# Performance work log

Measured on AMD Instinct MI355X. Metric: run time of the kernel, lower is better.

Reference implementation:

```python
import jax, jax.numpy as jnp
import numpy as np
from jax import lax

NB, HH, WW, C = 8, 64, 64, 192
G, K, DW_K, PA_K = 12, 3, 5, 3
GC, P = C // G, K * K
PAD, STRIDE, DIL = 1, 1, 1
OFFSET_SCALE = 1.0
LN_EPS = 1e-5


def _grid_sample(img, grid):
    # img: (B,Cc,H,W); grid: (B,L,P,2) xy in [-1,1]; bilinear, zeros padding, align_corners=False
    B, Cc, H, W = img.shape
    gx = (grid[..., 0] + 1.0) * (W * 0.5) - 0.5
    gy = (grid[..., 1] + 1.0) * (H * 0.5) - 0.5
    x0, y0 = jnp.floor(gx), jnp.floor(gy)

    def gather(xi, yi):
        valid = (xi >= 0) & (xi <= W - 1) & (yi >= 0) & (yi <= H - 1)
        xc = jnp.clip(xi, 0, W - 1).astype(jnp.int32)
        yc = jnp.clip(yi, 0, H - 1).astype(jnp.int32)
        v = jax.vmap(lambda im, y, x: im[:, y, x])(img, yc, xc)  # (B,Cc,L,P)
        return v * valid[:, None].astype(img.dtype)

    wx1, wy1 = gx - x0, gy - y0
    wx0, wy0 = 1.0 - wx1, 1.0 - wy1
    return (gather(x0, y0) * (wx0 * wy0)[:, None]
            + gather(x0 + 1.0, y0) * (wx1 * wy0)[:, None]
            + gather(x0, y0 + 1.0) * (wx0 * wy1)[:, None]
            + gather(x0 + 1.0, y0 + 1.0) * (wx1 * wy1)[:, None])


def _dcnv3_core(x, offset, mask):
    # x: (N,H,W,C) projected input; offset: (N,H,W,G*P*2); mask: (N,H,W,G*P)
    N, H, W, _ = x.shape
    xp = jnp.pad(x, ((0, 0), (PAD, PAD), (PAD, PAD), (0, 0)))
    Hp, Wp = H + 2 * PAD, W + 2 * PAD
    Ho, Wo = offset.shape[1], offset.shape[2]
    base = (DIL * (K - 1)) // 2 + 0.5
    ref_y = (base + jnp.arange(Ho) * STRIDE) / Hp
    ref_x = (base + jnp.arange(Wo) * STRIDE) / Wp
    ref = jnp.stack(jnp.broadcast_arrays(ref_x[None, :], ref_y[:, None]), -1)  # (Ho,Wo,2) xy
    start = -((DIL * (K - 1)) // 2)
    pts = (start + jnp.arange(K) * DIL).astype(x.dtype)
    gxg = jnp.broadcast_to((pts / Wp)[:, None], (K, K))  # w offset varies along dim0 (torch order)
    gyg = jnp.broadcast_to((pts / Hp)[None, :], (K, K))
    grid = jnp.tile(jnp.stack([gxg, gyg], -1).reshape(P, 2), (G, 1))  # (G*P,2)
    loc = ref[None, :, :, None, :] + grid * OFFSET_SCALE  # (1,Ho,Wo,G*P,2)
    norm = jnp.array([Wp, Hp], dtype=x.dtype)
    loc = loc + offset.reshape(N, Ho, Wo, G * P, 2) * OFFSET_SCALE / norm
    sg = 2.0 * loc - 1.0  # (N,Ho,Wo,G*P,2)
    img = xp.reshape(N, Hp * Wp, G, GC).transpose(0, 2, 3, 1).reshape(N * G, GC, Hp, Wp)
    grd = sg.reshape(N, Ho * Wo, G, P, 2).transpose(0, 2, 1, 3, 4).reshape(N * G, Ho * Wo, P, 2)
    samp = _grid_sample(img, grd)  # (N*G, GC, L, P)
    m = mask.reshape(N, Ho * Wo, G, P).transpose(0, 2, 1, 3).reshape(N * G, 1, Ho * Wo, P)
    out = (samp * m).sum(-1)  # (N*G, GC, L)
    return out.reshape(N, G, GC, Ho * Wo).transpose(0, 3, 1, 2).reshape(N, Ho, Wo, C)


def _dcnv3(x, dw_w, dw_b, ln_g, ln_b, off_w, off_b, msk_w, msk_b, in_w, in_b, out_w, out_b, cfs_w, cfs_b):
    N, H, W, _ = x.shape
    x_proj = x @ in_w + in_b
    # depthwise conv (5x5) -> LayerNorm (channels_last) -> GELU(exact)
    u = lax.conv_general_dilated(x, dw_w, (1, 1), 'SAME',
                                 dimension_numbers=('NHWC', 'HWIO', 'NHWC'),
                                 feature_group_count=C) + dw_b
    mu = u.mean(-1, keepdims=True)
    var = ((u - mu) ** 2).mean(-1, keepdims=True)
    u = (u - mu) * lax.rsqrt(var + LN_EPS) * ln_g + ln_b
    u = jax.nn.gelu(u, approximate=False)
    offset = u @ off_w + off_b  # (N,H,W,G*P*2)
    m = jax.nn.softmax((u @ msk_w + msk_b).reshape(N, H, W, G, P), axis=-1).reshape(N, H, W, G * P)
    y = _dcnv3_core(x_proj, offset, m)
    cfs = jax.nn.sigmoid(u @ cfs_w + cfs_b)  # (N,H,W,G)
    cfs = jnp.repeat(cfs, GC, axis=-1)       # (N,H,W,C), group-blockwise
    y = y * (1.0 - cfs) + x_proj * cfs
    return y @ out_w + out_b


def _patch_attention(x):
    # x: (N,H,W,C) -> std over softmax'd 3x3 neighbor scores: (N,H,W)
    N, H, W, _ = x.shape
    pad = (PA_K - 1) // 2
    xp = jnp.pad(x, ((0, 0), (pad, pad), (pad, pad), (0, 0)))
    neigh = jnp.stack([xp[:, i:i + H, j:j + W, :] for i in range(PA_K) for j in range(PA_K)],
                      axis=-1)  # (N,H,W,C,K1*K2), torch unfold ordering
    scores = jnp.einsum('nhwc,nhwck->nhwk', x, neigh)
    sm = jax.nn.softmax(scores, axis=-1)
    return jnp.std(sm, axis=-1, ddof=1)  # torch.std is unbiased


def setup_inputs() -> dict:
    key = jax.random.key(0)
    ks = jax.random.split(key, 8)
    s = 0.02
    return {
        'x': jax.random.normal(ks[0], (NB, HH, WW, C), jnp.float32),
        'dw_w': jax.random.normal(ks[1], (DW_K, DW_K, 1, C), jnp.float32) * s,
        'dw_b': jnp.zeros((C,), jnp.float32),
        'ln_g': jnp.ones((C,), jnp.float32),
        'ln_b': jnp.zeros((C,), jnp.float32),
        'off_w': jax.random.normal(ks[2], (C, G * P * 2), jnp.float32) * s,
        'off_b': jnp.zeros((G * P * 2,), jnp.float32),
        'msk_w': jax.random.normal(ks[3], (C, G * P), jnp.float32) * s,
        'msk_b': jnp.zeros((G * P,), jnp.float32),
        'in_w': jax.random.normal(ks[4], (C, C), jnp.float32) * s,
        'in_b': jnp.zeros((C,), jnp.float32),
        'out_w': jax.random.normal(ks[5], (C, C), jnp.float32) * s,
        'out_b': jnp.zeros((C,), jnp.float32),
        'cfs_w': jax.random.normal(ks[6], (C, G), jnp.float32) * s,
        'cfs_b': jnp.zeros((G,), jnp.float32),
    }


def reference(x, dw_w, dw_b, ln_g, ln_b, off_w, off_b, msk_w, msk_b, in_w, in_b, out_w, out_b, cfs_w, cfs_b):
    x1 = _dcnv3(x, dw_w, dw_b, ln_g, ln_b, off_w, off_b, msk_w, msk_b, in_w, in_b, out_w, out_b, cfs_w, cfs_b)
    mask = _patch_attention(x1)           # (N,H,W)
    return x + x1 * mask[..., None]
```

## Files before the change

### kernel.cpp

```cpp
#include <hip/hip_runtime.h>
#include <hip/hip_bf16.h>
#include <math.h>

#define NB 8
#define HH 64
#define WW 64
#define C 192
#define G 12
#define GC 16
#define P 9
#define NPIX (NB*HH*WW)

typedef __attribute__((ext_vector_type(8))) short short8;
typedef __attribute__((ext_vector_type(4))) float f32x4;
typedef unsigned short ushort;

__device__ __forceinline__ ushort to_bf16(float f) {
  __hip_bfloat16 b = __float2bfloat16(f);
  return *(ushort*)&b;
}
__device__ __forceinline__ float bf2f(ushort u) {
  union { unsigned u; float f; } cv; cv.u = ((unsigned)u) << 16; return cv.f;
}
__device__ __forceinline__ float bflo(unsigned u) {
  union { unsigned v; float f; } c; c.v = u << 16; return c.f;
}
__device__ __forceinline__ float bfhi(unsigned u) {
  union { unsigned v; float f; } c; c.v = u & 0xffff0000u; return c.f;
}

__global__ __launch_bounds__(256) void cvt_kernel(const float* __restrict__ in,
                                                  ushort* __restrict__ out) {
  int i = blockIdx.x*256 + threadIdx.x;
  float4 v0 = ((const float4*)in)[2*i];
  float4 v1 = ((const float4*)in)[2*i+1];
  short8 r;
  r[0]=to_bf16(v0.x); r[1]=to_bf16(v0.y); r[2]=to_bf16(v0.z); r[3]=to_bf16(v0.w);
  r[4]=to_bf16(v1.x); r[5]=to_bf16(v1.y); r[6]=to_bf16(v1.z); r[7]=to_bf16(v1.w);
  ((short8*)out)[i] = r;
}

__global__ void prep_w_kernel(const float* __restrict__ in_w, const float* __restrict__ out_w,
    const float* __restrict__ off_w, const float* __restrict__ msk_w, const float* __restrict__ cfs_w,
    const float* __restrict__ off_b, const float* __restrict__ msk_b, const float* __restrict__ cfs_b,
    ushort* __restrict__ in_wt, ushort* __restrict__ out_wt, ushort* __restrict__ wf_t,
    float* __restrict__ bf_bias) {
  int idx = blockIdx.x*256 + threadIdx.x;
  if (idx < 36864) {
    int n = idx/192, k = idx%192;
    in_wt[idx] = to_bf16(in_w[k*192 + n]);
  } else if (idx < 73728) {
    int j = idx - 36864; int n = j/192, k = j%192;
    out_wt[j] = to_bf16(out_w[k*192 + n]);
  } else if (idx < 147456) {
    int j = idx - 73728; int n = j/192, k = j%192;
    float v = 0.f;
    if (n < 216)      v = off_w[k*216 + n];
    else if (n < 324) v = msk_w[k*108 + (n-216)];
    else if (n < 336) v = cfs_w[k*12  + (n-324)];
    wf_t[j] = to_bf16(v);
  }
  if (idx < 384) {
    float b = 0.f;
    if (idx < 216)      b = off_b[idx];
    else if (idx < 324) b = msk_b[idx-216];
    else if (idx < 336) b = cfs_b[idx-324];
    bf_bias[idx] = b;
  }
}

template<int NW, int NSTORE, bool BF16OUT>
__global__ __launch_bounds__(256) void mfma_gemm(const ushort* __restrict__ A,
    const ushort* __restrict__ Wt, const float* __restrict__ bias,
    void* __restrict__ Cout_) {
  __shared__ ushort As[4*128*8];
  __shared__ ushort Bs[4*64*8];
  int pix0 = blockIdx.x * 128, n0 = blockIdx.y * 64;
  int tid = threadIdx.x;
  int wid = tid >> 6, lane = tid & 63;
  int lr = lane >> 4, lc = lane & 15;

  f32x4 acc[2][4];
  #pragma unroll
  for (int m=0;m<2;m++)
    #pragma unroll
    for (int j=0;j<4;j++) acc[m][j] = (f32x4){0.f,0.f,0.f,0.f};

  int sa0_kb = tid >> 7,        sa0_row = tid & 127;
  int sa1_kb = (tid+256) >> 7,  sa1_row = (tid+256) & 127;
  int sb_kb  = tid >> 6,        sb_n    = tid & 63;

  short8 pa0, pa1, pb;
  auto load_tile = [&](int k0) {
    pa0 = *(const short8*)&A[(size_t)(pix0 + sa0_row)*192 + k0 + sa0_kb*8];
    pa1 = *(const short8*)&A[(size_t)(pix0 + sa1_row)*192 + k0 + sa1_kb*8];
    pb  = *(const short8*)&Wt[(size_t)(n0 + sb_n)*192 + k0 + sb_kb*8];
  };
  load_tile(0);

  for (int t = 0; t < 6; t++) {
    __syncthreads();
    *(short8*)&As[(size_t)tid*8]        = pa0;
    *(short8*)&As[(size_t)(tid+256)*8]  = pa1;
    *(short8*)&Bs[(size_t)tid*8]        = pb;
    __syncthreads();
    if (t < 5) load_tile((t+1)*32);
    short8 a0 = *(const short8*)&As[(size_t)(lr*128 + wid*32 + lc)*8];
    short8 a1 = *(const short8*)&As[(size_t)(lr*128 + wid*32 + 16 + lc)*8];
    #pragma unroll
    for (int j=0;j<4;j++) {
      short8 b = *(const short8*)&Bs[(size_t)(lr*64 + j*16 + lc)*8];
      acc[0][j] = __builtin_amdgcn_mfma_f32_16x16x32_bf16(a0, b, acc[0][j], 0,0,0);
      acc[1][j] = __builtin_amdgcn_mfma_f32_16x16x32_bf16(a1, b, acc[1][j], 0,0,0);
    }
  }
  #pragma unroll
  for (int j=0;j<4;j++) {
    int col = n0 + j*16 + lc;
    if (NW != NSTORE && col >= NSTORE) continue;
    float bb = bias[col];
    #pragma unroll
    for (int m=0;m<2;m++) {
      size_t rbase = pix0 + wid*32 + m*16 + lr*4;
      #pragma unroll
      for (int r=0;r<4;r++) {
        float v = acc[m][j][r] + bb;
        if (BF16OUT) ((ushort*)Cout_)[(rbase + r)*NSTORE + col] = to_bf16(v);
        else         ((float*) Cout_)[(rbase + r)*NSTORE + col] = v;
      }
    }
  }
}

#define SEG 16
__global__ __launch_bounds__(192) void dw_ln_gelu_kernel(const float* __restrict__ x,
    const float* __restrict__ dw_w, const float* __restrict__ dw_b,
    const float* __restrict__ ln_g, const float* __restrict__ ln_b,
    ushort* __restrict__ u_out) {
  int blk = blockIdx.x;
  int qw = blk & 3; int nh = blk >> 2;
  int h = nh & 63, n = nh >> 6;
  int c = threadIdx.x;
  int w0 = qw * SEG;

  float kw[25];
  #pragma unroll
  for (int t=0;t<25;t++) kw[t] = dw_w[t*C + c];

  float acc[SEG];
  float bb = dw_b[c];
  #pragma unroll
  for (int i=0;i<SEG;i++) acc[i] = bb;

  #pragma unroll
  for (int i=0;i<5;i++) {
    int hy = h + i - 2;
    if (hy < 0 || hy >= HH) continue;
    const float* rowp = &x[(((size_t)n*HH + hy)*WW)*C + c];
    #pragma unroll
    for (int wi=0; wi<SEG+4; wi++) {
      int w_in = w0 - 2 + wi;
      if (w_in < 0 || w_in >= WW) continue;
      float v = rowp[(size_t)w_in*C];
      #pragma unroll
      for (int j=0;j<5;j++) {
        int a = wi - j;
        if (a >= 0 && a < SEG) acc[a] += v * kw[i*5+j];
      }
    }
  }

  __shared__ float lds_acc[SEG][C+1];
  __shared__ float part1[SEG][12], part2[SEG][12];
  __shared__ float mu_s[SEG], rs_s[SEG];
  #pragma unroll
  for (int i=0;i<SEG;i++) lds_acc[i][c] = acc[i];
  __syncthreads();
  {
    int p = threadIdx.x & 15, chunk = threadIdx.x >> 4;
    float s1 = 0.f, s2 = 0.f;
    #pragma unroll
    for (int k=0;k<16;k++) {
      float v = lds_acc[p][chunk*16 + k];
      s1 += v; s2 += v*v;
    }
    part1[p][chunk] = s1; part2[p][chunk] = s2;
  }
  __syncthreads();
  if (threadIdx.x < SEG) {
    int p = threadIdx.x;
    float t1 = 0.f, t2 = 0.f;
    #pragma unroll
    for (int k=0;k<12;k++){ t1 += part1[p][k]; t2 += part2[p][k]; }
    float mu = t1 * (1.0f/C);
    float var = t2 * (1.0f/C) - mu*mu;
    mu_s[p] = mu; rs_s[p] = rsqrtf(var + 1e-5f);
  }
  __syncthreads();
  float gg = ln_g[c], lb = ln_b[c];
  size_t obase = ((size_t)nh*WW + w0)*C + c;
  #pragma unroll
  for (int i=0;i<SEG;i++) {
    float uv = (acc[i] - mu_s[i])*rs_s[i]*gg + lb;
    uv = 0.5f*uv*(1.0f + erff(uv*0.70710678118654752f));
    u_out[obase + (size_t)i*C] = to_bf16(uv);
  }
}

#define SPX 4
__global__ __launch_bounds__(192) void sample_kernel(const ushort* __restrict__ omc,
    const ushort* __restrict__ x_proj, ushort* __restrict__ y_out) {
  int pix0 = blockIdx.x * SPX;
  int n = pix0 >> 12;
  int hw = pix0 & 4095; int h = hw >> 6; int w0 = hw & 63;
  int tid = threadIdx.x;
  __shared__ int   addrs[SPX*108*4];
  __shared__ float wts[SPX*108*4];
  __shared__ float msm[SPX][108];
  __shared__ float cfss[SPX][12];

  for (int i = tid; i < SPX*108; i += 192) {
    int px = i / 108, gp = i % 108;
    int p = gp % 9;
    const float pts[3] = {-1.f, 0.f, 1.f};
    unsigned off2 = ((const unsigned*)omc)[(size_t)(pix0+px)*168 + gp];
    float ox = bflo(off2), oy = bfhi(off2);
    float gx = 1.0f + (float)(w0+px) + pts[p/3] + ox;
    float gy = 1.0f + (float)h + pts[p%3] + oy;
    float x0f = floorf(gx), y0f = floorf(gy);
    float wx1 = gx - x0f, wy1 = gy - y0f;
    float wx0 = 1.f-wx1, wy0 = 1.f-wy1;
    int x0 = (int)x0f, y0 = (int)y0f;
    bool xv0 = (x0   >= 1) && (x0   <= 64);
    bool xv1 = (x0+1 >= 1) && (x0+1 <= 64);
    bool yv0 = (y0   >= 1) && (y0   <= 64);
    bool yv1 = (y0+1 >= 1) && (y0+1 <= 64);
    int base = n*HH*WW*C;
    int4 a4;
    a4.x = (yv0&&xv0) ? (base + ((y0-1)*WW + (x0-1))*C)*2 : 0;
    a4.y = (yv0&&xv1) ? (base + ((y0-1)*WW + (x0  ))*C)*2 : 0;
    a4.z = (yv1&&xv0) ? (base + ((y0  )*WW + (x0-1))*C)*2 : 0;
    a4.w = (yv1&&xv1) ? (base + ((y0  )*WW + (x0  ))*C)*2 : 0;
    ((int4*)addrs)[i] = a4;
    float4 w4;
    w4.x = (yv0&&xv0) ? wx0*wy0 : 0.f;
    w4.y = (yv0&&xv1) ? wx1*wy0 : 0.f;
    w4.z = (yv1&&xv0) ? wx0*wy1 : 0.f;
    w4.w = (yv1&&xv1) ? wx1*wy1 : 0.f;
    ((float4*)wts)[i] = w4;
  }
  if (tid < SPX*12) {
    int px = tid / 12, gg = tid % 12;
    const ushort* mrow = &omc[(size_t)(pix0+px)*336 + 216 + gg*9];
    float lv[P];
    #pragma unroll
    for (int p=0;p<P;p++) lv[p] = bf2f(mrow[p]);
    float m = -1e30f;
    #pragma unroll
    for (int p=0;p<P;p++) m = fmaxf(m, lv[p]);
    float e[P]; float s = 0.f;
    #pragma unroll
    for (int p=0;p<P;p++){ e[p] = expf(lv[p]-m); s += e[p]; }
    float inv = 1.0f/s;
    #pragma unroll
    for (int p=0;p<P;p++) msm[px][gg*9+p] = e[p]*inv;
  } else if (tid < SPX*12*2) {
    int q = tid - SPX*12;
    int px = q / 12, gg = q % 12;
    cfss[px][gg] = 1.0f/(1.0f+expf(-bf2f(omc[(size_t)(pix0+px)*336 + 324 + gg])));
  }
  __syncthreads();
  for (int i = tid; i < SPX*108; i += 192) {
    int px = i / 108, gp = i % 108;
    float m = msm[px][gp] * (1.0f - cfss[px][gp/9]);
    f32x4 w4 = *(f32x4*)&wts[i*4];
    w4 *= m;
    *(f32x4*)&wts[i*4] = w4;
  }
  __syncthreads();
  int px = tid / 48, s = tid - (tid/48)*48;
  int g = s >> 2;
  int cb = s * 8;
  const char* xb = (const char*)x_proj;
  float4 accY = {0.f,0.f,0.f,0.f};
  #pragma unroll
  for (int pb = 0; pb < 3; pb++) {
    uint2 q0_, q1_, q2_, q3_, q4_, q5_, q6_, q7_, q8_, q9_, qa_, qb_;
    float4 wv0, wv1, wv2;
    {
      int gp = g*9 + pb*3;
      int4 a0 = ((const int4*)addrs)[px*108+gp];
      int4 a1 = ((const int4*)addrs)[px*108+gp+1];
      int4 a2 = ((const int4*)addrs)[px*108+gp+2];
      wv0 = ((const float4*)wts)[px*108+gp];
      wv1 = ((const float4*)wts)[px*108+gp+1];
      wv2 = ((const float4*)wts)[px*108+gp+2];
      q0_ = *(const uint2*)(xb + (unsigned)(a0.x + cb));
      q1_ = *(const uint2*)(xb + (unsigned)(a0.y + cb));
      q2_ = *(const uint2*)(xb + (unsigned)(a0.z + cb));
      q3_ = *(const uint2*)(xb + (unsigned)(a0.w + cb));
      q4_ = *(const uint2*)(xb + (unsigned)(a1.x + cb));
      q5_ = *(const uint2*)(xb + (unsigned)(a1.y + cb));
      q6_ = *(const uint2*)(xb + (unsigned)(a1.z + cb));
      q7_ = *(const uint2*)(xb + (unsigned)(a1.w + cb));
      q8_ = *(const uint2*)(xb + (unsigned)(a2.x + cb));
      q9_ = *(const uint2*)(xb + (unsigned)(a2.y + cb));
      qa_ = *(const uint2*)(xb + (unsigned)(a2.z + cb));
      qb_ = *(const uint2*)(xb + (unsigned)(a2.w + cb));
    }
    accY.x += wv0.x*bflo(q0_.x) + wv0.y*bflo(q1_.x) + wv0.z*bflo(q2_.x) + wv0.w*bflo(q3_.x);
    accY.y += wv0.x*bfhi(q0_.x) + wv0.y*bfhi(q1_.x) + wv0.z*bfhi(q2_.x) + wv0.w*bfhi(q3_.x);
    accY.z += wv0.x*bflo(q0_.y) + wv0.y*bflo(q1_.y) + wv0.z*bflo(q2_.y) + wv0.w*bflo(q3_.y);
    accY.w += wv0.x*bfhi(q0_.y) + wv0.y*bfhi(q1_.y) + wv0.z*bfhi(q2_.y) + wv0.w*bfhi(q3_.y);
    accY.x += wv1.x*bflo(q4_.x) + wv1.y*bflo(q5_.x) + wv1.z*bflo(q6_.x) + wv1.w*bflo(q7_.x);
    accY.y += wv1.x*bfhi(q4_.x) + wv1.y*bfhi(q5_.x) + wv1.z*bfhi(q6_.x) + wv1.w*bfhi(q7_.x);
    accY.z += wv1.x*bflo(q4_.y) + wv1.y*bflo(q5_.y) + wv1.z*bflo(q6_.y) + wv1.w*bflo(q7_.y);
    accY.w += wv1.x*bfhi(q4_.y) + wv1.y*bfhi(q5_.y) + wv1.z*bfhi(q6_.y) + wv1.w*bfhi(q7_.y);
    accY.x += wv2.x*bflo(q8_.x) + wv2.y*bflo(q9_.x) + wv2.z*bflo(qa_.x) + wv2.w*bflo(qb_.x);
    accY.y += wv2.x*bfhi(q8_.x) + wv2.y*bfhi(q9_.x) + wv2.z*bfhi(qa_.x) + wv2.w*bfhi(qb_.x);
    accY.z += wv2.x*bflo(q8_.y) + wv2.y*bflo(q9_.y) + wv2.z*bflo(qa_.y) + wv2.w*bflo(qb_.y);
    accY.w += wv2.x*bfhi(q8_.y) + wv2.y*bfhi(q9_.y) + wv2.z*bfhi(qa_.y) + wv2.w*bfhi(qb_.y);
  }
  float cf = cfss[px][g];
  uint2 qx = *(const uint2*)(xb + ((size_t)(pix0+px)*C)*2 + cb);
  accY.x += bflo(qx.x)*cf;
  accY.y += bfhi(qx.x)*cf;
  accY.z += bflo(qx.y)*cf;
  accY.w += bfhi(qx.y)*cf;
  ushort4 r;
  r.x = to_bf16(accY.x); r.y = to_bf16(accY.y);
  r.z = to_bf16(accY.z); r.w = to_bf16(accY.w);
  *(ushort4*)&y_out[(size_t)(pix0+px)*C + s*4] = r;
}

__global__ __launch_bounds__(256) void pattn_kernel(const float* __restrict__ x,
    const ushort* __restrict__ x1, float* __restrict__ out) {
  __shared__ unsigned xs[100*97];
  __shared__ float psc[64][36];
  __shared__ float sd_s[64];
  int blk = blockIdx.x;
  int n = blk >> 6;
  int ty = (blk >> 3) & 7, tx = blk & 7;
  int th0 = ty*8, tw0 = tx*8;
  int tid = threadIdx.x;
  const unsigned* x1u = (const unsigned*)x1;
  for (int i = tid; i < 100*96; i += 256) {
    int cell = i / 96, wd = i - cell*96;
    int gy = th0 - 1 + cell/10, gx = tw0 - 1 + cell%10;
    unsigned v = 0;
    if (gy>=0 && gy<HH && gx>=0 && gx<WW)
      v = x1u[(((size_t)n*HH+gy)*WW+gx)*96 + wd];
    xs[cell*97 + wd] = v;
  }
  __syncthreads();
  {
    int px = tid >> 2, qq = tid & 3;
    int py = px >> 3, pxx = px & 7;
    int cell = (py+1)*10 + (pxx+1);
    float cen[48];
    #pragma unroll
    for (int k=0;k<24;k++) {
      unsigned w = xs[cell*97 + qq*24 + k];
      cen[2*k] = bflo(w); cen[2*k+1] = bfhi(w);
    }
    #pragma unroll
    for (int ni=0;ni<9;ni++) {
      int nc = cell + (ni/3-1)*10 + (ni%3-1);
      float a = 0.f;
      #pragma unroll
      for (int k=0;k<24;k++) {
        unsigned w = xs[nc*97 + qq*24 + k];
        a += cen[2*k]*bflo(w) + cen[2*k+1]*bfhi(w);
      }
      psc[px][qq*9+ni] = a;
    }
  }
  __syncthreads();
  if (tid < 64) {
    float sc[9];
    #pragma unroll
    for (int k=0;k<9;k++)
      sc[k] = psc[tid][k] + psc[tid][9+k] + psc[tid][18+k] + psc[tid][27+k];
    float m = sc[0];
    #pragma unroll
    for (int k=1;k<9;k++) m = fmaxf(m, sc[k]);
    float pr[9]; float s = 0.f;
    #pragma unroll
    for (int k=0;k<9;k++){ pr[k] = expf(sc[k]-m); s += pr[k]; }
    float inv = 1.0f/s;
    float mean = 0.f;
    #pragma unroll
    for (int k=0;k<9;k++){ pr[k] *= inv; mean += pr[k]; }
    mean *= (1.0f/9.0f);
    float var = 0.f;
    #pragma unroll
    for (int k=0;k<9;k++){ float d = pr[k]-mean; var += d*d; }
    sd_s[tid] = sqrtf(var*(1.0f/8.0f));
  }
  __syncthreads();
  for (int i = tid; i < 64*96; i += 256) {
    int p2 = i / 96, wd = i - p2*96;
    int py2 = p2 >> 3, px2 = p2 & 7;
    unsigned v = xs[((py2+1)*10 + (px2+1))*97 + wd];
    size_t pix = ((size_t)n*HH + th0+py2)*WW + tw0+px2;
    float2 xv = ((const float2*)x)[pix*96 + wd];
    float sd = sd_s[p2];
    float2 o; o.x = xv.x + bflo(v)*sd; o.y = xv.y + bfhi(v)*sd;
    ((float2*)out)[pix*96 + wd] = o;
  }
}

extern "C" void kernel_launch(void* const* d_in, const int* in_sizes, int n_in,
                              void* d_out, int out_size, void* d_ws, size_t ws_size,
                              hipStream_t stream) {
  const float* x     = (const float*)d_in[0];
  const float* dw_w  = (const float*)d_in[1];
  const float* dw_b  = (const float*)d_in[2];
  const float* ln_g  = (const float*)d_in[3];
  const float* ln_b  = (const float*)d_in[4];
  const float* off_w = (const float*)d_in[5];
  const float* off_b = (const float*)d_in[6];
  const float* msk_w = (const float*)d_in[7];
  const float* msk_b = (const float*)d_in[8];
  const float* in_w  = (const float*)d_in[9];
  const float* in_b  = (const float*)d_in[10];
  const float* out_w = (const float*)d_in[11];
  const float* out_b = (const float*)d_in[12];
  const float* cfs_w = (const float*)d_in[13];
  const float* cfs_b = (const float*)d_in[14];
  float* outp = (float*)d_out;

  ushort* omc    = (ushort*)d_ws;
  ushort* xproj  = omc + (size_t)NPIX*336;
  ushort* x_bf   = xproj + (size_t)NPIX*192;
  ushort* u_bf   = x_bf + (size_t)NPIX*192;
  ushort* in_wt  = u_bf + (size_t)NPIX*192;
  ushort* out_wt = in_wt + 192*192;
  ushort* wf_t   = out_wt + 192*192;
  float*  bfb    = (float*)(wf_t + 384*192);

  cvt_kernel<<<NPIX*192/8/256, 256, 0, stream>>>(x, x_bf);
  prep_w_kernel<<<(147456+255)/256, 256, 0, stream>>>(in_w, out_w, off_w, msk_w, cfs_w,
                                                       off_b, msk_b, cfs_b,
                                                       in_wt, out_wt, wf_t, bfb);
  mfma_gemm<192,192,true><<<dim3(NPIX/128, 3), 256, 0, stream>>>(x_bf, in_wt, in_b, xproj);
  dw_ln_gelu_kernel<<<NB*HH*4, 192, 0, stream>>>(x, dw_w, dw_b, ln_g, ln_b, u_bf);
  mfma_gemm<384,336,true><<<dim3(NPIX/128, 6), 256, 0, stream>>>(u_bf, wf_t, bfb, omc);
  sample_kernel<<<NPIX/SPX, 192, 0, stream>>>(omc, xproj, u_bf);
  mfma_gemm<192,192,true><<<dim3(NPIX/128, 3), 256, 0, stream>>>(u_bf, out_wt, out_b, x_bf);
  pattn_kernel<<<NB*64, 256, 0, stream>>>(x, x_bf, outp);
}
```

Measured before the change: 158.4 us.

## Fuse fp32-to-bf16 input conversion into GEMM and widen sampler per-thread channels

```diff
diff --git a/kernel.cpp b/kernel.cpp
--- a/kernel.cpp
+++ b/kernel.cpp
@@ -27,17 +27,6 @@
 }
 __device__ __forceinline__ float bfhi(unsigned u) {
   union { unsigned v; float f; } c; c.v = u & 0xffff0000u; return c.f;
-}
-
-__global__ __launch_bounds__(256) void cvt_kernel(const float* __restrict__ in,
-                                                  ushort* __restrict__ out) {
-  int i = blockIdx.x*256 + threadIdx.x;
-  float4 v0 = ((const float4*)in)[2*i];
-  float4 v1 = ((const float4*)in)[2*i+1];
-  short8 r;
-  r[0]=to_bf16(v0.x); r[1]=to_bf16(v0.y); r[2]=to_bf16(v0.z); r[3]=to_bf16(v0.w);
-  r[4]=to_bf16(v1.x); r[5]=to_bf16(v1.y); r[6]=to_bf16(v1.z); r[7]=to_bf16(v1.w);
-  ((short8*)out)[i] = r;
 }
 
 __global__ void prep_w_kernel(const float* __restrict__ in_w, const float* __restrict__ out_w,
@@ -69,8 +58,8 @@
   }
 }
 
-template<int NW, int NSTORE, bool BF16OUT>
-__global__ __launch_bounds__(256) void mfma_gemm(const ushort* __restrict__ A,
+template<int NW, int NSTORE, bool BF16OUT, bool AF32>
+__global__ __launch_bounds__(256) void mfma_gemm(const void* __restrict__ A_,
     const ushort* __restrict__ Wt, const float* __restrict__ bias,
     void* __restrict__ Cout_) {
   __shared__ ushort As[4*128*8];
@@ -92,8 +81,21 @@
 
   short8 pa0, pa1, pb;
   auto load_tile = [&](int k0) {
-    pa0 = *(const short8*)&A[(size_t)(pix0 + sa0_row)*192 + k0 + sa0_kb*8];
-    pa1 = *(const short8*)&A[(size_t)(pix0 + sa1_row)*192 + k0 + sa1_kb*8];
+    if (AF32) {
+      const float* Af = (const float*)A_;
+      float4 u0 = *(const float4*)&Af[(size_t)(pix0 + sa0_row)*192 + k0 + sa0_kb*8];
+      float4 u1 = *(const float4*)&Af[(size_t)(pix0 + sa0_row)*192 + k0 + sa0_kb*8 + 4];
+      pa0[0]=to_bf16(u0.x); pa0[1]=to_bf16(u0.y); pa0[2]=to_bf16(u0.z); pa0[3]=to_bf16(u0.w);
+      pa0[4]=to_bf16(u1.x); pa0[5]=to_bf16(u1.y); pa0[6]=to_bf16(u1.z); pa0[7]=to_bf16(u1.w);
+      float4 v0 = *(const float4*)&Af[(size_t)(pix0 + sa1_row)*192 + k0 + sa1_kb*8];
+      float4 v1 = *(const float4*)&Af[(size_t)(pix0 + sa1_row)*192 + k0 + sa1_kb*8 + 4];
+      pa1[0]=to_bf16(v0.x); pa1[1]=to_bf16(v0.y); pa1[2]=to_bf16(v0.z); pa1[3]=to_bf16(v0.w);
+      pa1[4]=to_bf16(v1.x); pa1[5]=to_bf16(v1.y); pa1[6]=to_bf16(v1.z); pa1[7]=to_bf16(v1.w);
+    } else {
+      const ushort* Ab = (const ushort*)A_;
+      pa0 = *(const short8*)&Ab[(size_t)(pix0 + sa0_row)*192 + k0 + sa0_kb*8];
+      pa1 = *(const short8*)&Ab[(size_t)(pix0 + sa1_row)*192 + k0 + sa1_kb*8];
+    }
     pb  = *(const short8*)&Wt[(size_t)(n0 + sb_n)*192 + k0 + sb_kb*8];
   };
   load_tile(0);
@@ -207,7 +209,13 @@
   }
 }
 
-#define SPX 4
+#define SPX 8
+__device__ __forceinline__ void fma8(float* acc, float w, uint4 q) {
+  acc[0] += w*bflo(q.x); acc[1] += w*bfhi(q.x);
+  acc[2] += w*bflo(q.y); acc[3] += w*bfhi(q.y);
+  acc[4] += w*bflo(q.z); acc[5] += w*bfhi(q.z);
+  acc[6] += w*bflo(q.w); acc[7] += w*bfhi(q.w);
+}
 __global__ __launch_bounds__(192) void sample_kernel(const ushort* __restrict__ omc,
     const ushort* __restrict__ x_proj, ushort* __restrict__ y_out) {
   int pix0 = blockIdx.x * SPX;
@@ -264,7 +272,7 @@
     float inv = 1.0f/s;
     #pragma unroll
     for (int p=0;p<P;p++) msm[px][gg*9+p] = e[p]*inv;
-  } else if (tid < SPX*12*2) {
+  } else {
     int q = tid - SPX*12;
     int px = q / 12, gg = q % 12;
     cfss[px][gg] = 1.0f/(1.0f+expf(-bf2f(omc[(size_t)(pix0+px)*336 + 324 + gg])));
@@ -278,59 +286,46 @@
     *(f32x4*)&wts[i*4] = w4;
   }
   __syncthreads();
-  int px = tid / 48, s = tid - (tid/48)*48;
-  int g = s >> 2;
-  int cb = s * 8;
+  int px = tid / 24, s = tid - (tid/24)*24;
+  int g = s >> 1;
+  int cb = s * 16;
   const char* xb = (const char*)x_proj;
-  float4 accY = {0.f,0.f,0.f,0.f};
+  float acc[8] = {0.f,0.f,0.f,0.f,0.f,0.f,0.f,0.f};
   #pragma unroll
   for (int pb = 0; pb < 3; pb++) {
-    uint2 q0_, q1_, q2_, q3_, q4_, q5_, q6_, q7_, q8_, q9_, qa_, qb_;
-    float4 wv0, wv1, wv2;
-    {
-      int gp = g*9 + pb*3;
-      int4 a0 = ((const int4*)addrs)[px*108+gp];
-      int4 a1 = ((const int4*)addrs)[px*108+gp+1];
-      int4 a2 = ((const int4*)addrs)[px*108+gp+2];
-      wv0 = ((const float4*)wts)[px*108+gp];
-      wv1 = ((const float4*)wts)[px*108+gp+1];
-      wv2 = ((const float4*)wts)[px*108+gp+2];
-      q0_ = *(const uint2*)(xb + (unsigned)(a0.x + cb));
-      q1_ = *(const uint2*)(xb + (unsigned)(a0.y + cb));
-      q2_ = *(const uint2*)(xb + (unsigned)(a0.z + cb));
-      q3_ = *(const uint2*)(xb + (unsigned)(a0.w + cb));
-      q4_ = *(const uint2*)(xb + (unsigned)(a1.x + cb));
-      q5_ = *(const uint2*)(xb + (unsigned)(a1.y + cb));
-      q6_ = *(const uint2*)(xb + (unsigned)(a1.z + cb));
-      q7_ = *(const uint2*)(xb + (unsigned)(a1.w + cb));
-      q8_ = *(const uint2*)(xb + (unsigned)(a2.x + cb));
-      q9_ = *(const uint2*)(xb + (unsigned)(a2.y + cb));
-      qa_ = *(const uint2*)(xb + (unsigned)(a2.z + cb));
-      qb_ = *(const uint2*)(xb + (unsigned)(a2.w + cb));
-    }
-    accY.x += wv0.x*bflo(q0_.x) + wv0.y*bflo(q1_.x) + wv0.z*bflo(q2_.x) + wv0.w*bflo(q3_.x);
-    accY.y += wv0.x*bfhi(q0_.x) + wv0.y*bfhi(q1_.x) + wv0.z*bfhi(q2_.x) + wv0.w*bfhi(q3_.x);
-    accY.z += wv0.x*bflo(q0_.y) + wv0.y*bflo(q1_.y) + wv0.z*bflo(q2_.y) + wv0.w*bflo(q3_.y);
-    accY.w += wv0.x*bfhi(q0_.y) + wv0.y*bfhi(q1_.y) + wv0.z*bfhi(q2_.y) + wv0.w*bfhi(q3_.y);
-    accY.x += wv1.x*bflo(q4_.x) + wv1.y*bflo(q5_.x) + wv1.z*bflo(q6_.x) + wv1.w*bflo(q7_.x);
-    accY.y += wv1.x*bfhi(q4_.x) + wv1.y*bfhi(q5_.x) + wv1.z*bfhi(q6_.x) + wv1.w*bfhi(q7_.x);
-    accY.z += wv1.x*bflo(q4_.y) + wv1.y*bflo(q5_.y) + wv1.z*bflo(q6_.y) + wv1.w*bflo(q7_.y);
-    accY.w += wv1.x*bfhi(q4_.y) + wv1.y*bfhi(q5_.y) + wv1.z*bfhi(q6_.y) + wv1.w*bfhi(q7_.y);
-    accY.x += wv2.x*bflo(q8_.x) + wv2.y*bflo(q9_.x) + wv2.z*bflo(qa_.x) + wv2.w*bflo(qb_.x);
-    accY.y += wv2.x*bfhi(q8_.x) + wv2.y*bfhi(q9_.x) + wv2.z*bfhi(qa_.x) + wv2.w*bfhi(qb_.x);
-    accY.z += wv2.x*bflo(q8_.y) + wv2.y*bflo(q9_.y) + wv2.z*bflo(qa_.y) + wv2.w*bflo(qb_.y);
-    accY.w += wv2.x*bfhi(q8_.y) + wv2.y*bfhi(q9_.y) + wv2.z*bfhi(qa_.y) + wv2.w*bfhi(qb_.y);
+    int gp = g*9 + pb*3;
+    int4 a0 = ((const int4*)addrs)[px*108+gp];
+    int4 a1 = ((const int4*)addrs)[px*108+gp+1];
+    int4 a2 = ((const int4*)addrs)[px*108+gp+2];
+    float4 wv0 = ((const float4*)wts)[px*108+gp];
+    float4 wv1 = ((const float4*)wts)[px*108+gp+1];
+    float4 wv2 = ((const float4*)wts)[px*108+gp+2];
+    uint4 t00 = *(const uint4*)(xb + (unsigned)(a0.x + cb));
+    uint4 t01 = *(const uint4*)(xb + (unsigned)(a0.y + cb));
+    uint4 t02 = *(const uint4*)(xb + (unsigned)(a0.z + cb));
+    uint4 t03 = *(const uint4*)(xb + (unsigned)(a0.w + cb));
+    uint4 t10 = *(const uint4*)(xb + (unsigned)(a1.x + cb));
+    uint4 t11 = *(const uint4*)(xb + (unsigned)(a1.y + cb));
+    uint4 t12 = *(const uint4*)(xb + (unsigned)(a1.z + cb));
+    uint4 t13 = *(const uint4*)(xb + (unsigned)(a1.w + cb));
+    uint4 t20 = *(const uint4*)(xb + (unsigned)(a2.x + cb));
+    uint4 t21 = *(const uint4*)(xb + (unsigned)(a2.y + cb));
+    uint4 t22 = *(const uint4*)(xb + (unsigned)(a2.z + cb));
+    uint4 t23 = *(const uint4*)(xb + (unsigned)(a2.w + cb));
+    fma8(acc, wv0.x, t00); fma8(acc, wv0.y, t01);
+    fma8(acc, wv0.z, t02); fma8(acc, wv0.w, t03);
+    fma8(acc, wv1.x, t10); fma8(acc, wv1.y, t11);
+    fma8(acc, wv1.z, t12); fma8(acc, wv1.w, t13);
+    fma8(acc, wv2.x, t20); fma8(acc, wv2.y, t21);
+    fma8(acc, wv2.z, t22); fma8(acc, wv2.w, t23);
   }
   float cf = cfss[px][g];
-  uint2 qx = *(const uint2*)(xb + ((size_t)(pix0+px)*C)*2 + cb);
-  accY.x += bflo(qx.x)*cf;
-  accY.y += bfhi(qx.x)*cf;
-  accY.z += bflo(qx.y)*cf;
-  accY.w += bfhi(qx.y)*cf;
-  ushort4 r;
-  r.x = to_bf16(accY.x); r.y = to_bf16(accY.y);
-  r.z = to_bf16(accY.z); r.w = to_bf16(accY.w);
-  *(ushort4*)&y_out[(size_t)(pix0+px)*C + s*4] = r;
+  uint4 qx = *(const uint4*)(xb + ((size_t)(pix0+px)*C)*2 + cb);
+  fma8(acc, cf, qx);
+  short8 r;
+  #pragma unroll
+  for (int k=0;k<8;k++) r[k] = to_bf16(acc[k]);
+  *(short8*)&y_out[(size_t)(pix0+px)*C + s*8] = r;
 }
 
 __global__ __launch_bounds__(256) void pattn_kernel(const float* __restrict__ x,
@@ -432,21 +427,20 @@
 
   ushort* omc    = (ushort*)d_ws;
   ushort* xproj  = omc + (size_t)NPIX*336;
-  ushort* x_bf   = xproj + (size_t)NPIX*192;
-  ushort* u_bf   = x_bf + (size_t)NPIX*192;
+  ushort* x1_bf  = xproj + (size_t)NPIX*192;
+  ushort* u_bf   = x1_bf + (size_t)NPIX*192;
   ushort* in_wt  = u_bf + (size_t)NPIX*192;
   ushort* out_wt = in_wt + 192*192;
   ushort* wf_t   = out_wt + 192*192;
   float*  bfb    = (float*)(wf_t + 384*192);
 
-  cvt_kernel<<<NPIX*192/8/256, 256, 0, stream>>>(x, x_bf);
   prep_w_kernel<<<(147456+255)/256, 256, 0, stream>>>(in_w, out_w, off_w, msk_w, cfs_w,
                                                        off_b, msk_b, cfs_b,
                                                        in_wt, out_wt, wf_t, bfb);
-  mfma_gemm<192,192,true><<<dim3(NPIX/128, 3), 256, 0, stream>>>(x_bf, in_wt, in_b, xproj);
+  mfma_gemm<192,192,true,true><<<dim3(NPIX/128, 3), 256, 0, stream>>>(x, in_wt, in_b, xproj);
   dw_ln_gelu_kernel<<<NB*HH*4, 192, 0, stream>>>(x, dw_w, dw_b, ln_g, ln_b, u_bf);
-  mfma_gemm<384,336,true><<<dim3(NPIX/128, 6), 256, 0, stream>>>(u_bf, wf_t, bfb, omc);
+  mfma_gemm<384,336,true,false><<<dim3(NPIX/128, 6), 256, 0, stream>>>(u_bf, wf_t, bfb, omc);
   sample_kernel<<<NPIX/SPX, 192, 0, stream>>>(omc, xproj, u_bf);
-  mfma_gemm<192,192,true><<<dim3(NPIX/128, 3), 256, 0, stream>>>(u_bf, out_wt, out_b, x_bf);
-  pattn_kernel<<<NB*64, 256, 0, stream>>>(x, x_bf, outp);
-}
+  mfma_gemm<192,192,true,false><<<dim3(NPIX/128, 3), 256, 0, stream>>>(u_bf, out_wt, out_b, x1_bf);
+  pattn_kernel<<<NB*64, 256, 0, stream>>>(x, x1_bf, outp);
+}
```

New measurement: 155.3 us. 2.0% less time.
